# Optimization experiments

Measured on AMD Instinct MI355X. Metric: run time of the kernel, lower is better.

## Reference

```python
import jax, jax.numpy as jnp
import numpy as np

B, S, H, D = 4, 1024, 16, 64
DIM = H * D          # 1024
FF_INNER = 4 * DIM   # 4096
ROT_BASE = 1000.0


def _l2norm(x):
    # F.normalize(p=2, dim=-1): x / max(||x||_2, 1e-12)
    n = jnp.linalg.norm(x, axis=-1, keepdims=True)
    return x / jnp.maximum(n, 1e-12)


def _rmsnorm(x):
    return x * jax.lax.rsqrt(jnp.mean(x * x, axis=-1, keepdims=True) + jnp.finfo(jnp.float32).eps)


def _rope_tables(seq, d, base):
    inv_freq = base ** (-(jnp.arange(0, d, 2, dtype=jnp.float32) / d))
    freqs = jnp.outer(jnp.arange(seq, dtype=jnp.float32), inv_freq)  # [S, D/2]
    # original caches cos/sin in bfloat16
    cos = jnp.cos(freqs).astype(jnp.bfloat16)[None, :, None, :]
    sin = jnp.sin(freqs).astype(jnp.bfloat16)[None, :, None, :]
    return cos, sin


def _rope(x, cos, sin):
    d = x.shape[3] // 2
    x1, x2 = x[..., :d], x[..., d:]
    y1 = x1 * cos + x2 * sin
    y2 = -x1 * sin + x2 * cos
    return jnp.concatenate([y1, y2], axis=3).astype(x.dtype)


def setup_inputs() -> dict:
    key = jax.random.key(0)
    ks = jax.random.split(key, 12)
    w = lambda k, shp: 0.02 * jax.random.normal(k, shp, dtype=jnp.float32)
    inp = {
        'h_states': jax.random.normal(ks[0], (B, S, DIM), dtype=jnp.float32),
        'attention_mask': jnp.tril(jnp.ones((S, S), dtype=jnp.float32))[None].repeat(B, axis=0),
        'Wq': w(ks[1], (DIM, DIM)), 'Wk': w(ks[2], (DIM, DIM)), 'Wv': w(ks[3], (DIM, DIM)),
        'WqB': w(ks[4], (DIM, DIM)), 'WkB': w(ks[5], (DIM, DIM)),
        'Wo': w(ks[6], (DIM, DIM)), 'bo': jnp.zeros((DIM,), jnp.float32),
        'Wff_in': w(ks[7], (DIM, 2 * FF_INNER)), 'bff_in': jnp.zeros((2 * FF_INNER,), jnp.float32),
        'Wff_out': w(ks[8], (FF_INNER, DIM)), 'bff_out': jnp.zeros((DIM,), jnp.float32),
        'learnedlambda': jnp.asarray(1.0, jnp.float32),
        'l2normscale': jnp.log(jnp.asarray(float(S) ** 2 - float(S), jnp.float32)),
    }
    return inp


def reference(h_states, attention_mask, Wq, Wk, Wv, WqB, WkB, Wo, bo,
              Wff_in, bff_in, Wff_out, bff_out, learnedlambda, l2normscale):
    inner = _rmsnorm(h_states)                               # layerwisenorm (rmsnorm, no affine)
    scale = D ** -0.5

    def proj(Wm):
        return (inner @ Wm).reshape(B, S, H, D)
    q, k, v = proj(Wq), proj(Wk), proj(Wv)
    bq, bk = proj(WqB), proj(WkB)

    cos, sin = _rope_tables(S, D, ROT_BASE)
    q = _rope(_l2norm(q), cos, sin)
    k = _rope(_l2norm(k), cos, sin)
    bq = _rope(_l2norm(bq), cos, sin)
    bk = _rope(_l2norm(bk), cos, sin)

    # main branch: causal softmax attention, scale=1, scaled by learned l2normscale
    scores = jnp.einsum('bihd,bjhd->bhij', q, k)             # [B,H,S,S]
    causal = jnp.tril(jnp.ones((S, S), dtype=bool))
    scores = jnp.where(causal, scores, -jnp.inf)
    attn = jax.nn.softmax(scores, axis=-1)
    y = l2normscale * jnp.einsum('bhij,bjhd->bihd', attn, v)  # [B,S,H,D]

    # bias branch: softmax-free masked scores @ ones == row-sum broadcast over D
    bscores = jnp.einsum('bihd,bjhd->bhij', bq, bk) * scale
    bscores = bscores * attention_mask[:, None, :, :]
    brow = bscores.sum(axis=-1)                               # [B,H,S]
    y = y + jnp.transpose(brow, (0, 2, 1))[..., None]         # broadcast over D

    attn_out = y.reshape(B, S, DIM) @ Wo + bo

    # SwiGLU FFN: chunk -> x, gate; silu(gate) * x
    u = inner @ Wff_in + bff_in
    xh, gate = jnp.split(u, 2, axis=-1)
    dense_out = (jax.nn.silu(gate) * xh) @ Wff_out + bff_out

    return h_states * learnedlambda + dense_out + attn_out
```

## Files before the change

### kernel.cpp

```cpp
#include <hip/hip_runtime.h>
#include <stdint.h>
#include <math.h>

typedef float f32x4 __attribute__((ext_vector_type(4)));
typedef short s16x8 __attribute__((ext_vector_type(8)));
typedef unsigned short bfu;

#define AS1q const __attribute__((address_space(1))) void*
#define AS3q __attribute__((address_space(3))) void*

static __device__ __forceinline__ float bf2f(bfu v) {
  return __uint_as_float(((unsigned int)v) << 16);
}
static __device__ __forceinline__ bfu f2bf(float f) {
  unsigned int u = __float_as_uint(f);
  return (bfu)((u + 0x7fffu + ((u >> 16) & 1u)) >> 16);
}

struct PreArgs {
  const float* w5[5];
  const float* Wffin;
  const float* Wffout;
  const float* Wo;
  const float* h;
  bfu* wt5; bfu* wtfi; bfu* wtfoc;
  bfu* cosb; bfu* sinb; bfu* inner;
};
__global__ __launch_bounds__(256) void prologue_k(PreArgs a) {
  __shared__ float shmem[32 * 33];
  int id = blockIdx.x;
  if (id < 18432) {
    const float* W; bfu* Wt; int K, N, dstride, dofs, mode, nb, kb;
    if (id < 5120) {
      int z = id >> 10, rem = id & 1023;
      W = a.w5[z]; Wt = a.wt5 + ((size_t)z << 20);
      K = 1024; N = 1024; dstride = 1024; dofs = 0; mode = 0;
      nb = (rem & 31) << 5; kb = (rem >> 5) << 5;
    } else if (id < 13312) {
      int id2 = id - 5120;
      W = a.Wffin; Wt = a.wtfi; K = 1024; N = 8192; dstride = 1024; dofs = 0; mode = 1;
      nb = (id2 & 255) << 5; kb = (id2 >> 8) << 5;
    } else if (id < 17408) {
      int id3 = id - 13312;
      W = a.Wffout; Wt = a.wtfoc; K = 4096; N = 1024; dstride = 5120; dofs = 0; mode = 2;
      nb = (id3 & 31) << 5; kb = (id3 >> 5) << 5;
    } else {
      int id4 = id - 17408;
      W = a.Wo; Wt = a.wtfoc; K = 1024; N = 1024; dstride = 5120; dofs = 4096; mode = 2;
      nb = (id4 & 31) << 5; kb = (id4 >> 5) << 5;
    }
    float (*t)[33] = reinterpret_cast<float(*)[33]>(shmem);
    int tx = threadIdx.x & 31, ty = threadIdx.x >> 5;
#pragma unroll
    for (int i = 0; i < 4; i++) {
      int r = ty + i * 8;
      t[r][tx] = W[(size_t)(kb + r) * N + nb + tx];
    }
    __syncthreads();
#pragma unroll
    for (int i = 0; i < 4; i++) {
      int r = ty + i * 8;
      int n = nb + r;
      int nd = n;
      if (mode == 1) { int j = n & 4095, isg = n >> 12; nd = ((j >> 4) << 5) | (isg << 4) | (j & 15); }
      int k = kb + tx;
      int kp = (mode == 2) ? (((k >> 5) << 5) | ((k & 15) << 1) | ((k >> 4) & 1)) : k;
      Wt[(size_t)nd * dstride + dofs + kp] = f2bf(t[tx][r]);
    }
  } else if (id < 18560) {
    int idx = (id - 18432) * 256 + threadIdx.x;
    int s = idx >> 5, i = idx & 31;
    float f = powf(1000.0f, -(float)i / 32.0f);
    float fr = (float)s * f;
    a.cosb[idx] = f2bf(cosf(fr));
    a.sinb[idx] = f2bf(sinf(fr));
  } else {
    int row = id - 18560;
    const float* hr = a.h + (size_t)row * 1024;
    f32x4 x = *reinterpret_cast<const f32x4*>(hr + threadIdx.x * 4);
    float ss = x[0] * x[0] + x[1] * x[1] + x[2] * x[2] + x[3] * x[3];
    for (int off = 32; off; off >>= 1) ss += __shfl_down(ss, off);
    int wave = threadIdx.x >> 6, lane = threadIdx.x & 63;
    if (lane == 0) shmem[wave] = ss;
    __syncthreads();
    float tot = shmem[0] + shmem[1] + shmem[2] + shmem[3];
    float r = rsqrtf(tot * (1.0f / 1024.0f) + 1.1920929e-07f);
    bfu* o = a.inner + (size_t)row * 1024 + threadIdx.x * 4;
    o[0] = f2bf(x[0] * r); o[1] = f2bf(x[1] * r);
    o[2] = f2bf(x[2] * r); o[3] = f2bf(x[3] * r);
  }
}

template <int EPI>
__global__ __launch_bounds__(512, 2) void gemm256p(const bfu* __restrict__ A, const bfu* __restrict__ Bt,
                                                   bfu* __restrict__ outB,
                                                   const float* __restrict__ bias,
                                                   int M, int N, int K, int rbm, int rbn) {
  __shared__ __align__(16) char lds[131072];
  int nbx = N >> 8;
  int c = blockIdx.x & 7, rr = blockIdx.x >> 3;
  int ca = nbx / rbn;
  int bn0 = (c % ca) * rbn, bm0 = (c / ca) * rbm;
  int bm = bm0 + rr / rbn, bn = bn0 + rr % rbn;
  int tid = threadIdx.x, w = tid >> 6, lane = tid & 63;
  int wm = w >> 2, wn = w & 3;
  int g = lane >> 4, l15 = lane & 15;
  int NT = K >> 6;
  int NI = NT >> 1;

  f32x4 acc[8][4];
#pragma unroll
  for (int m = 0; m < 8; m++)
#pragma unroll
    for (int n = 0; n < 4; n++) acc[m][n] = (f32x4){0.f, 0.f, 0.f, 0.f};

  s16x8 af[4][2];
  s16x8 bfr[4][2];

  auto stage = [&](int mat, int kt, int hf) {
    if (kt >= NT) return;
    int d = kt & 1;
    const bfu* s0 = (mat == 0) ? A : Bt;
    int rowbase = ((mat == 0) ? bm : bn) * 256 + hf * 128;
    int k0 = kt << 6;
    char* base = lds + d * 65536 + mat * 32768 + hf * 16384;
#pragma unroll
    for (int r = 0; r < 2; r++) {
      int L = r * 512 + tid;
      int row = L >> 3, cc = L & 7;
      int kc = cc ^ (row & 7);
      const bfu* src = s0 + (size_t)(rowbase + row) * K + k0 + kc * 8;
      char* dst = base + r * 8192 + w * 1024;
      __builtin_amdgcn_global_load_lds((AS1q)src, (AS3q)dst, 16, 0, 0);
    }
  };

  auto ldA = [&](int d, int mh) {
    const char* base = lds + d * 65536 + wm * 16384;
#pragma unroll
    for (int mm = 0; mm < 4; mm++) {
      int row = mh * 64 + mm * 16 + l15;
#pragma unroll
      for (int ks = 0; ks < 2; ks++)
        af[mm][ks] = *reinterpret_cast<const s16x8*>(
            base + row * 128 + (((ks * 4 + g) ^ (row & 7)) << 4));
    }
  };
  auto ldB2 = [&](int d, int nh) {
    const char* base = lds + d * 65536 + 32768 + (wn >> 1) * 16384;
#pragma unroll
    for (int nn = 0; nn < 2; nn++) {
      int row = (wn & 1) * 64 + (nh * 2 + nn) * 16 + l15;
#pragma unroll
      for (int ks = 0; ks < 2; ks++)
        bfr[nh * 2 + nn][ks] = *reinterpret_cast<const s16x8*>(
            base + row * 128 + (((ks * 4 + g) ^ (row & 7)) << 4));
    }
  };
  auto mfma_q = [&](int mh, int nh) {
    asm volatile("s_waitcnt lgkmcnt(0)" ::: "memory");
    __builtin_amdgcn_sched_barrier(0);
    __builtin_amdgcn_s_barrier();
    __builtin_amdgcn_s_setprio(1);
#pragma unroll
    for (int mm = 0; mm < 4; mm++)
#pragma unroll
      for (int nn = 0; nn < 2; nn++) {
        int n = nh * 2 + nn, m = mh * 4 + mm;
#pragma unroll
        for (int ks = 0; ks < 2; ks++)
          acc[m][n] = __builtin_amdgcn_mfma_f32_16x16x32_bf16(af[mm][ks], bfr[n][ks], acc[m][n], 0, 0, 0);
      }
    __builtin_amdgcn_s_setprio(0);
    __builtin_amdgcn_sched_barrier(0);
  };

  stage(1, 0, 0); stage(0, 0, 0); stage(0, 0, 1); stage(1, 0, 1);
  stage(1, 1, 0); stage(1, 1, 1);
  asm volatile("s_waitcnt vmcnt(4)" ::: "memory");
  __builtin_amdgcn_s_barrier();
  __builtin_amdgcn_sched_barrier(0);

  for (int i = 0; i < NI; i++) {
    int t0 = 2 * i, t1 = 2 * i + 1;
    bool last = (i == NI - 1);
    ldA(0, 0); ldB2(0, 0);
    stage(0, t1, 0);
    mfma_q(0, 0);
    ldB2(0, 1);
    stage(0, t1, 1);
    mfma_q(0, 1);
    ldA(0, 1);
    stage(1, t0 + 2, 0);
    mfma_q(1, 0);
    stage(1, t0 + 2, 1);
    mfma_q(1, 1);
    if (last) { asm volatile("s_waitcnt vmcnt(0)" ::: "memory"); }
    else      { asm volatile("s_waitcnt vmcnt(4)" ::: "memory"); }
    __builtin_amdgcn_s_barrier();
    __builtin_amdgcn_sched_barrier(0);
    ldA(1, 0); ldB2(1, 0);
    stage(0, t0 + 2, 0);
    mfma_q(0, 0);
    ldB2(1, 1);
    stage(0, t0 + 2, 1);
    mfma_q(0, 1);
    ldA(1, 1);
    stage(1, t1 + 2, 0);
    mfma_q(1, 0);
    stage(1, t1 + 2, 1);
    mfma_q(1, 1);
    asm volatile("s_waitcnt vmcnt(4)" ::: "memory");
    __builtin_amdgcn_s_barrier();
    __builtin_amdgcn_sched_barrier(0);
  }

  int j0 = (bn * 8 + wn * 2) * 16 + l15;
  float bx0 = bias[j0], bg0 = bias[j0 + 4096];
  float bx1 = bias[j0 + 16], bg1 = bias[j0 + 16 + 4096];
  int cb = (bn * 4 + wn) * 32 + 2 * l15;
#pragma unroll
  for (int m = 0; m < 8; m++) {
#pragma unroll
    for (int r = 0; r < 4; r++) {
      int row = bm * 256 + wm * 128 + m * 16 + g * 4 + r;
      float xh0 = acc[m][0][r] + bx0, gt0 = acc[m][1][r] + bg0;
      float xh1 = acc[m][2][r] + bx1, gt1 = acc[m][3][r] + bg1;
      float s0 = gt0 / (1.0f + __expf(-gt0)) * xh0;
      float s1 = gt1 / (1.0f + __expf(-gt1)) * xh1;
      unsigned int pk = (unsigned int)f2bf(s0) | ((unsigned int)f2bf(s1) << 16);
      *reinterpret_cast<unsigned int*>(outB + (size_t)row * 5120 + cb) = pk;
    }
  }
}

__global__ __launch_bounds__(256, 3) void gemm128p(const bfu* __restrict__ A, const bfu* __restrict__ Bt,
                                                   bfu* __restrict__ qb, bfu* __restrict__ kb,
                                                   bfu* __restrict__ vT,
                                                   bfu* __restrict__ bqh, bfu* __restrict__ bkh,
                                                   const bfu* __restrict__ ct, const bfu* __restrict__ st,
                                                   int M, int N, int K, int rbm, int rbn) {
  __shared__ __align__(16) char lds[49152];
  int nbx = N >> 7;
  int c = blockIdx.x & 7, rr = blockIdx.x >> 3;
  int ca = nbx / rbn;
  int bn0 = (c % ca) * rbn, bm0 = (c / ca) * rbm;
  int bm = bm0 + rr / rbn, bn = bn0 + rr % rbn;
  int tid = threadIdx.x, w = tid >> 6, lane = tid & 63;
  int wm = w >> 1, wn = w & 1;
  int g = lane >> 4, l15 = lane & 15;
  int NT = K >> 5;

  f32x4 acc[4][4];
#pragma unroll
  for (int m = 0; m < 4; m++)
#pragma unroll
    for (int n = 0; n < 4; n++) acc[m][n] = (f32x4){0.f, 0.f, 0.f, 0.f};

  auto stage = [&](int buf, int t) {
    int k0 = t << 5;
#pragma unroll
    for (int r = 0; r < 2; r++) {
      int L = r * 256 + tid;
      int row = L >> 2, cc = L & 3;
      int kc = cc ^ (row & 3);
      const bfu* srcA = A + (size_t)(bm * 128 + row) * K + k0 + kc * 8;
      char* dstA = lds + buf * 16384 + r * 4096 + w * 1024;
      __builtin_amdgcn_global_load_lds((AS1q)srcA, (AS3q)dstA, 16, 0, 0);
      const bfu* srcB = Bt + (size_t)(bn * 128 + row) * K + k0 + kc * 8;
      char* dstB = lds + buf * 16384 + 8192 + r * 4096 + w * 1024;
      __builtin_amdgcn_global_load_lds((AS1q)srcB, (AS3q)dstB, 16, 0, 0);
    }
  };

  stage(0, 0); stage(1, 1);
  asm volatile("s_waitcnt vmcnt(4)" ::: "memory");
  __builtin_amdgcn_s_barrier();
  __builtin_amdgcn_sched_barrier(0);

  int bc = 0;
  for (int t = 0; t < NT; t++) {
    int bs = bc + 2; if (bs >= 3) bs -= 3;
    if (t + 2 < NT) stage(bs, t + 2);
    const char* la = lds + bc * 16384;
    const char* lb = la + 8192;
    s16x8 af[4], bfr[4];
#pragma unroll
    for (int m = 0; m < 4; m++) {
      int row = wm * 64 + m * 16 + l15;
      af[m] = *reinterpret_cast<const s16x8*>(la + row * 64 + ((g ^ (row & 3)) << 4));
    }
#pragma unroll
    for (int n = 0; n < 4; n++) {
      int row = wn * 64 + n * 16 + l15;
      bfr[n] = *reinterpret_cast<const s16x8*>(lb + row * 64 + ((g ^ (row & 3)) << 4));
    }
    asm volatile("s_waitcnt lgkmcnt(0)" ::: "memory");
    __builtin_amdgcn_sched_barrier(0);
    __builtin_amdgcn_s_setprio(1);
#pragma unroll
    for (int m = 0; m < 4; m++)
#pragma unroll
      for (int n = 0; n < 4; n++)
        acc[m][n] = __builtin_amdgcn_mfma_f32_16x16x32_bf16(af[m], bfr[n], acc[m][n], 0, 0, 0);
    __builtin_amdgcn_s_setprio(0);
    __builtin_amdgcn_sched_barrier(0);
    if (t < NT - 2) { asm volatile("s_waitcnt vmcnt(4)" ::: "memory"); }
    else            { asm volatile("s_waitcnt vmcnt(0)" ::: "memory"); }
    __builtin_amdgcn_s_barrier();
    __builtin_amdgcn_sched_barrier(0);
    bc++; if (bc == 3) bc = 0;
  }

  int which = bn >> 3;
  int hh = (bn & 7) * 2 + wn;
  if (which == 2) {
    bfu* lv = reinterpret_cast<bfu*>(lds);
#pragma unroll
    for (int m = 0; m < 4; m++) {
#pragma unroll
      for (int r = 0; r < 4; r++) {
        int sl = wm * 64 + m * 16 + g * 4 + r;
#pragma unroll
        for (int j = 0; j < 4; j++) {
          int d = j * 16 + l15;
          lv[(wn * 64 + d) * 136 + sl] = f2bf(acc[m][j][r]);
        }
      }
    }
    __syncthreads();
    int b = bm >> 3, h0 = (bn & 7) * 2;
#pragma unroll
    for (int i = 0; i < 8; i++) {
      int linear = i * 256 + tid;
      int hw = linear >> 10, rem = linear & 1023;
      int d = rem >> 4, sl8 = (rem & 15) << 3;
      s16x8 v8 = *reinterpret_cast<const s16x8*>(&lv[(hw * 64 + d) * 136 + sl8]);
      size_t dstofs = (((size_t)((b << 4) + h0 + hw) << 6) + d) * 1024 + (bm & 7) * 128 + sl8;
      *reinterpret_cast<s16x8*>(vT + dstofs) = v8;
    }
  } else {
#pragma unroll
    for (int m = 0; m < 4; m++) {
#pragma unroll
      for (int r = 0; r < 4; r++) {
        int row = bm * 128 + wm * 64 + m * 16 + g * 4 + r;
        int s = row & 1023, b = row >> 10;
        float a0 = acc[m][0][r], a1 = acc[m][1][r];
        float a2 = acc[m][2][r], a3 = acc[m][3][r];
        float ss = a0 * a0 + a1 * a1 + a2 * a2 + a3 * a3;
        ss += __shfl_xor(ss, 1); ss += __shfl_xor(ss, 2);
        ss += __shfl_xor(ss, 4); ss += __shfl_xor(ss, 8);
        float inv = 1.0f / fmaxf(sqrtf(ss), 1e-12f);
        float xn0 = a0 * inv, xn1 = a1 * inv, xn2 = a2 * inv, xn3 = a3 * inv;
        float c0 = bf2f(ct[(s << 5) + l15]),      s0v = bf2f(st[(s << 5) + l15]);
        float c1 = bf2f(ct[(s << 5) + 16 + l15]), s1v = bf2f(st[(s << 5) + 16 + l15]);
        float o0 = xn0 * c0 + xn2 * s0v;
        float o1 = xn1 * c1 + xn3 * s1v;
        float o2 = xn2 * c0 - xn0 * s0v;
        float o3 = xn3 * c1 - xn1 * s1v;
        unsigned long long pk =
            (unsigned long long)((unsigned int)f2bf(o0) | ((unsigned int)f2bf(o1) << 16)) |
            ((unsigned long long)((unsigned int)f2bf(o2) | ((unsigned int)f2bf(o3) << 16)) << 32);
        size_t base = ((((size_t)((b << 4) + hh) << 10) + s) << 6) + (l15 << 2);
        bfu* dst = (which == 0) ? qb : (which == 1) ? kb : (which == 3) ? bqh : bkh;
        *reinterpret_cast<unsigned long long*>(dst + base) = pk;
      }
    }
  }
}

__global__ __launch_bounds__(256, 3) void gemm128f(const bfu* __restrict__ A, const bfu* __restrict__ Bt,
                                                   float* __restrict__ out,
                                                   const float* __restrict__ b1,
                                                   const float* __restrict__ b2,
                                                   const float* __restrict__ lam,
                                                   const float* __restrict__ h,
                                                   int M, int N, int K, int rbm, int rbn) {
  __shared__ __align__(16) char lds[98304];
  int nbx = N >> 7;
  int c = blockIdx.x & 7, rr = blockIdx.x >> 3;
  int ca = nbx / rbn;
  int bn0 = (c % ca) * rbn, bm0 = (c / ca) * rbm;
  int bm = bm0 + rr / rbn, bn = bn0 + rr % rbn;
  int tid = threadIdx.x, w = tid >> 6, lane = tid & 63;
  int wm = w >> 1, wn = w & 1;
  int g = lane >> 4, l15 = lane & 15;
  int NT = K >> 6;

  f32x4 acc[4][4];
#pragma unroll
  for (int m = 0; m < 4; m++)
#pragma unroll
    for (int n = 0; n < 4; n++) acc[m][n] = (f32x4){0.f, 0.f, 0.f, 0.f};

  auto stage = [&](int buf, int t) {
    int k0 = t << 6;
#pragma unroll
    for (int r = 0; r < 4; r++) {
      int L = r * 256 + tid;
      int row = L >> 3, cc = L & 7;
      int kc = cc ^ (row & 7);
      const bfu* srcA = A + (size_t)(bm * 128 + row) * K + k0 + kc * 8;
      char* dstA = lds + buf * 32768 + r * 4096 + w * 1024;
      __builtin_amdgcn_global_load_lds((AS1q)srcA, (AS3q)dstA, 16, 0, 0);
    }
#pragma unroll
    for (int r = 0; r < 4; r++) {
      int L = r * 256 + tid;
      int row = L >> 3, cc = L & 7;
      int kc = cc ^ (row & 7);
      const bfu* srcB = Bt + (size_t)(bn * 128 + row) * K + k0 + kc * 8;
      char* dstB = lds + buf * 32768 + 16384 + r * 4096 + w * 1024;
      __builtin_amdgcn_global_load_lds((AS1q)srcB, (AS3q)dstB, 16, 0, 0);
    }
  };

  stage(0, 0); stage(1, 1);
  asm volatile("s_waitcnt vmcnt(8)" ::: "memory");
  __builtin_amdgcn_s_barrier();
  __builtin_amdgcn_sched_barrier(0);

  int bc = 0;
  for (int t = 0; t < NT; t++) {
    int bs = bc + 2; if (bs >= 3) bs -= 3;
    if (t + 2 < NT) stage(bs, t + 2);
    const char* la = lds + bc * 32768;
    const char* lb = la + 16384;
    s16x8 af[4][2], bfr[4][2];
#pragma unroll
    for (int m = 0; m < 4; m++) {
      int row = wm * 64 + m * 16 + l15;
#pragma unroll
      for (int ks = 0; ks < 2; ks++)
        af[m][ks] = *reinterpret_cast<const s16x8*>(
            la + row * 128 + (((ks * 4 + g) ^ (row & 7)) << 4));
    }
#pragma unroll
    for (int n = 0; n < 4; n++) {
      int row = wn * 64 + n * 16 + l15;
#pragma unroll
      for (int ks = 0; ks < 2; ks++)
        bfr[n][ks] = *reinterpret_cast<const s16x8*>(
            lb + row * 128 + (((ks * 4 + g) ^ (row & 7)) << 4));
    }
    asm volatile("s_waitcnt lgkmcnt(0)" ::: "memory");
    __builtin_amdgcn_sched_barrier(0);
    __builtin_amdgcn_s_setprio(1);
#pragma unroll
    for (int m = 0; m < 4; m++)
#pragma unroll
      for (int n = 0; n < 4; n++)
#pragma unroll
        for (int ks = 0; ks < 2; ks++)
          acc[m][n] = __builtin_amdgcn_mfma_f32_16x16x32_bf16(af[m][ks], bfr[n][ks], acc[m][n], 0, 0, 0);
    __builtin_amdgcn_s_setprio(0);
    __builtin_amdgcn_sched_barrier(0);
    if (t < NT - 2) { asm volatile("s_waitcnt vmcnt(8)" ::: "memory"); }
    else            { asm volatile("s_waitcnt vmcnt(0)" ::: "memory"); }
    __builtin_amdgcn_s_barrier();
    __builtin_amdgcn_sched_barrier(0);
    bc++; if (bc == 3) bc = 0;
  }

  float lv = lam[0];
#pragma unroll
  for (int m = 0; m < 4; m++) {
    int row = bm * 128 + wm * 64 + m * 16 + g * 4;
#pragma unroll
    for (int n = 0; n < 4; n++) {
      int col = bn * 128 + wn * 64 + n * 16 + l15;
      float bb = b1[col] + b2[col];
#pragma unroll
      for (int r = 0; r < 4; r++) {
        size_t o = (size_t)(row + r) * 1024 + col;
        out[o] = acc[m][n][r] + bb + lv * h[o];
      }
    }
  }
}

__global__ __launch_bounds__(512) void brow_all(const bfu* __restrict__ bq, const bfu* __restrict__ bk,
                                                float* __restrict__ brow) {
  __shared__ float csums[8][64];
  int bh = blockIdx.x;
  int wave = threadIdx.x >> 6, lane = threadIdx.x & 63;
  size_t base = ((size_t)bh * 1024 + wave * 128) * 64 + lane;
  float s = 0.f;
  for (int j = 0; j < 128; j++) s += bf2f(bk[base + (size_t)j * 64]);
  csums[wave][lane] = s;
  __syncthreads();
  float p = 0.f;
  for (int cc = 0; cc < wave; cc++) p += csums[cc][lane];
  for (int j = 0; j < 128; j++) {
    p += bf2f(bk[base + (size_t)j * 64]);
    float t = bf2f(bq[base + (size_t)j * 64]) * p;
#pragma unroll
    for (int m2 = 1; m2 < 64; m2 <<= 1) t += __shfl_xor(t, m2);
    if (lane == 0) brow[bh * 1024 + wave * 128 + j] = 0.125f * t;
  }
}

__global__ __launch_bounds__(256) void flash_k(const bfu* __restrict__ q, const bfu* __restrict__ k,
                                               const bfu* __restrict__ vT,
                                               const float* __restrict__ brow,
                                               const float* __restrict__ l2p,
                                               bfu* __restrict__ y) {
  __shared__ __align__(16) bfu P[4][2][16][72];
  int id = blockIdx.x;
  int sub = id & 255;
  int qt = (id >> 8) ? 7 - (sub >> 6) : (sub >> 6);
  int bh = sub & 63;
  int wave = threadIdx.x >> 6, lane = threadIdx.x & 63;
  int g = lane >> 4, l15 = lane & 15;
  const size_t bhofs = (size_t)bh << 16;
  int rt0 = qt * 128 + wave * 32;

  s16x8 aq[2][2];
#pragma unroll
  for (int m = 0; m < 2; m++)
#pragma unroll
    for (int ks = 0; ks < 2; ks++)
      aq[m][ks] = *reinterpret_cast<const s16x8*>(
          q + bhofs + (size_t)(rt0 + m * 16 + l15) * 64 + ks * 32 + g * 8);

  f32x4 O[2][4];
  float mr[2][4], lr[2][4];
#pragma unroll
  for (int m = 0; m < 2; m++)
#pragma unroll
    for (int r = 0; r < 4; r++) { O[m][r] = (f32x4){0.f, 0.f, 0.f, 0.f}; mr[m][r] = -3.0e38f; lr[m][r] = 0.f; }

  s16x8 kA[4][2], kB[4][2];
  auto loadK = [&](s16x8 (&kd)[4][2], int jt) {
#pragma unroll
    for (int nt = 0; nt < 4; nt++)
#pragma unroll
      for (int ks = 0; ks < 2; ks++)
        kd[nt][ks] = *reinterpret_cast<const s16x8*>(
            k + bhofs + (size_t)(jt * 64 + nt * 16 + l15) * 64 + ks * 32 + g * 8);
  };

  int njt = 2 * qt + 2;
  loadK(kA, 0);

  auto body = [&](int jt, s16x8 (&kc)[4][2], s16x8 (&kn)[4][2], bool pf) {
    s16x8 vv[4][2];
#pragma unroll
    for (int nt = 0; nt < 4; nt++)
#pragma unroll
      for (int ks = 0; ks < 2; ks++)
        vv[nt][ks] = *reinterpret_cast<const s16x8*>(
            vT + ((size_t)(bh * 64 + nt * 16 + l15) << 10) + jt * 64 + ks * 32 + g * 8);

    bool act[2] = { jt * 64 <= rt0 + 15, jt * 64 <= rt0 + 31 };
    f32x4 sfr[2][4];
#pragma unroll
    for (int m = 0; m < 2; m++) {
      if (!act[m]) continue;
#pragma unroll
      for (int nt = 0; nt < 4; nt++) {
        sfr[m][nt] = (f32x4){0.f, 0.f, 0.f, 0.f};
#pragma unroll
        for (int ks = 0; ks < 2; ks++)
          sfr[m][nt] = __builtin_amdgcn_mfma_f32_16x16x32_bf16(aq[m][ks], kc[nt][ks], sfr[m][nt], 0, 0, 0);
      }
    }
    if (pf) loadK(kn, jt + 1);

#pragma unroll
    for (int m = 0; m < 2; m++) {
      if (!act[m]) continue;
      int rtm = rt0 + m * 16;
      if (jt * 64 + 63 > rtm) {
#pragma unroll
        for (int ntn = 0; ntn < 4; ntn++)
#pragma unroll
          for (int r = 0; r < 4; r++)
            if (jt * 64 + ntn * 16 + l15 > rtm + g * 4 + r) sfr[m][ntn][r] = -1e30f;
      }
      float alpha[4];
#pragma unroll
      for (int r = 0; r < 4; r++) {
        float v = fmaxf(fmaxf(sfr[m][0][r], sfr[m][1][r]), fmaxf(sfr[m][2][r], sfr[m][3][r]));
#pragma unroll
        for (int m2 = 1; m2 < 16; m2 <<= 1) v = fmaxf(v, __shfl_xor(v, m2));
        float mn = fmaxf(mr[m][r], v);
        alpha[r] = __expf(mr[m][r] - mn);
        mr[m][r] = mn;
      }
#pragma unroll
      for (int r = 0; r < 4; r++) {
        float rs = 0.f;
#pragma unroll
        for (int ntn = 0; ntn < 4; ntn++) {
          float e = __expf(sfr[m][ntn][r] - mr[m][r]);
          rs += e;
          P[wave][m][g * 4 + r][ntn * 16 + l15] = f2bf(e);
        }
#pragma unroll
        for (int m2 = 1; m2 < 16; m2 <<= 1) rs += __shfl_xor(rs, m2);
        lr[m][r] = lr[m][r] * alpha[r] + rs;
#pragma unroll
        for (int ntn = 0; ntn < 4; ntn++) O[m][ntn][r] *= alpha[r];
      }
    }
    asm volatile("s_waitcnt lgkmcnt(0)" ::: "memory");
    __builtin_amdgcn_sched_barrier(0);
#pragma unroll
    for (int m = 0; m < 2; m++) {
      if (!act[m]) continue;
      s16x8 pa[2];
#pragma unroll
      for (int ks = 0; ks < 2; ks++)
        pa[ks] = *reinterpret_cast<const s16x8*>(&P[wave][m][l15][ks * 32 + g * 8]);
#pragma unroll
      for (int nt = 0; nt < 4; nt++)
#pragma unroll
        for (int ks = 0; ks < 2; ks++)
          O[m][nt] = __builtin_amdgcn_mfma_f32_16x16x32_bf16(pa[ks], vv[nt][ks], O[m][nt], 0, 0, 0);
    }
  };

  for (int jt = 0; jt < njt; jt += 2) {
    body(jt, kA, kB, true);
    body(jt + 1, kB, kA, jt + 2 < njt);
  }

  float l2ns = l2p[0];
  int b = bh >> 4, hq = bh & 15;
#pragma unroll
  for (int m = 0; m < 2; m++)
#pragma unroll
    for (int r = 0; r < 4; r++) {
      int rowg = rt0 + m * 16 + g * 4 + r;
      float br = brow[bh * 1024 + rowg];
      float sc = l2ns / lr[m][r];
      float v0 = O[m][0][r] * sc + br;
      float v1 = O[m][1][r] * sc + br;
      float v2 = O[m][2][r] * sc + br;
      float v3 = O[m][3][r] * sc + br;
      unsigned int p01 = (unsigned int)f2bf(v0) | ((unsigned int)f2bf(v1) << 16);
      unsigned int p23 = (unsigned int)f2bf(v2) | ((unsigned int)f2bf(v3) << 16);
      size_t base = (size_t)(b * 1024 + rowg) * 5120 + 4096 + hq * 64;
      *reinterpret_cast<unsigned int*>(y + base + 2 * l15) = p01;
      *reinterpret_cast<unsigned int*>(y + base + 32 + 2 * l15) = p23;
    }
}

extern "C" void kernel_launch(void* const* d_in, const int* in_sizes, int n_in,
                              void* d_out, int out_size, void* d_ws, size_t ws_size,
                              hipStream_t stream) {
  const float* h      = (const float*)d_in[0];
  const float* Wq     = (const float*)d_in[2];
  const float* Wk     = (const float*)d_in[3];
  const float* Wv     = (const float*)d_in[4];
  const float* WqB    = (const float*)d_in[5];
  const float* WkB    = (const float*)d_in[6];
  const float* Wo     = (const float*)d_in[7];
  const float* bo     = (const float*)d_in[8];
  const float* Wffin  = (const float*)d_in[9];
  const float* bffin  = (const float*)d_in[10];
  const float* Wffout = (const float*)d_in[11];
  const float* bffout = (const float*)d_in[12];
  const float* lam    = (const float*)d_in[13];
  const float* l2ns   = (const float*)d_in[14];
  float* out = (float*)d_out;

  char* ws = (char*)d_ws;
  size_t off = 0;
  auto alloc = [&](size_t bytes) { void* p = ws + off; off += bytes; return p; };
  bfu* wt5   = (bfu*)alloc(5ull * 1024 * 1024 * 2);
  bfu* wtfi  = (bfu*)alloc(8192ull * 1024 * 2);
  bfu* wtfoc = (bfu*)alloc(1024ull * 5120 * 2);
  bfu* cosb  = (bfu*)alloc(1024ull * 32 * 2);
  bfu* sinb  = (bfu*)alloc(1024ull * 32 * 2);
  bfu* inner = (bfu*)alloc(4096ull * 1024 * 2);
  bfu* qb    = (bfu*)alloc(64ull * 1024 * 64 * 2);
  bfu* kb    = (bfu*)alloc(64ull * 1024 * 64 * 2);
  bfu* vtb   = (bfu*)alloc(64ull * 1024 * 64 * 2);
  bfu* bqh   = (bfu*)alloc(64ull * 1024 * 64 * 2);
  bfu* bkh   = (bfu*)alloc(64ull * 1024 * 64 * 2);
  float* browb = (float*)alloc(64ull * 1024 * 4);
  bfu* AB    = (bfu*)alloc(4096ull * 5120 * 2);

  PreArgs pa;
  pa.w5[0] = Wq; pa.w5[1] = Wk; pa.w5[2] = Wv; pa.w5[3] = WqB; pa.w5[4] = WkB;
  pa.Wffin = Wffin; pa.Wffout = Wffout; pa.Wo = Wo; pa.h = h;
  pa.wt5 = wt5; pa.wtfi = wtfi; pa.wtfoc = wtfoc;
  pa.cosb = cosb; pa.sinb = sinb; pa.inner = inner;
  prologue_k<<<dim3(22656), 256, 0, stream>>>(pa);

  gemm128p<<<dim3(1280), 256, 0, stream>>>(inner, wt5, qb, kb, vtb, bqh, bkh, cosb, sinb,
                                           4096, 5120, 1024, 32, 5);

  brow_all<<<dim3(64), 512, 0, stream>>>(bqh, bkh, browb);

  flash_k<<<dim3(512), 256, 0, stream>>>(qb, kb, vtb, browb, l2ns, AB);

  gemm256p<1><<<dim3(512), 512, 0, stream>>>(inner, wtfi, AB, bffin,
                                             4096, 8192, 1024, 8, 8);

  gemm128f<<<dim3(256), 256, 0, stream>>>(AB, wtfoc, out, bffout, bo, lam, h,
                                          4096, 1024, 5120, 8, 4);
}
```

Baseline: 322.6 us.

## Halve flash attention query tile to 64 rows and double grid size

The flash attention kernel now gives each wave 16 query rows instead of 32, so a block covers 64 rows and the grid doubles to 1024 blocks. Query tiles are ordered in a four-way zigzag to balance causal work. This raises parallelism and shrinks the per-wave register footprint and causal-mask waste. In exchange each block loads K and V for half as many query rows, which doubles K/V traffic per unit of work.

```diff
diff --git a/kernel.cpp b/kernel.cpp
--- a/kernel.cpp
+++ b/kernel.cpp
@@ -506,30 +506,27 @@
                                                const float* __restrict__ brow,
                                                const float* __restrict__ l2p,
                                                bfu* __restrict__ y) {
-  __shared__ __align__(16) bfu P[4][2][16][72];
+  __shared__ __align__(16) bfu P[4][16][72];
   int id = blockIdx.x;
   int sub = id & 255;
-  int qt = (id >> 8) ? 7 - (sub >> 6) : (sub >> 6);
-  int bh = sub & 63;
+  int a = sub >> 6, bh = sub & 63;
+  int quad = id >> 8;
+  int qt = (quad == 0) ? a : (quad == 1) ? 7 - a : (quad == 2) ? 8 + a : 15 - a;
   int wave = threadIdx.x >> 6, lane = threadIdx.x & 63;
   int g = lane >> 4, l15 = lane & 15;
   const size_t bhofs = (size_t)bh << 16;
-  int rt0 = qt * 128 + wave * 32;
-
-  s16x8 aq[2][2];
-#pragma unroll
-  for (int m = 0; m < 2; m++)
-#pragma unroll
-    for (int ks = 0; ks < 2; ks++)
-      aq[m][ks] = *reinterpret_cast<const s16x8*>(
-          q + bhofs + (size_t)(rt0 + m * 16 + l15) * 64 + ks * 32 + g * 8);
-
-  f32x4 O[2][4];
-  float mr[2][4], lr[2][4];
-#pragma unroll
-  for (int m = 0; m < 2; m++)
-#pragma unroll
-    for (int r = 0; r < 4; r++) { O[m][r] = (f32x4){0.f, 0.f, 0.f, 0.f}; mr[m][r] = -3.0e38f; lr[m][r] = 0.f; }
+  int rt0 = qt * 64 + wave * 16;
+
+  s16x8 aq[2];
+#pragma unroll
+  for (int ks = 0; ks < 2; ks++)
+    aq[ks] = *reinterpret_cast<const s16x8*>(
+        q + bhofs + (size_t)(rt0 + l15) * 64 + ks * 32 + g * 8);
+
+  f32x4 O[4];
+  float mr[4], lr[4];
+#pragma unroll
+  for (int r = 0; r < 4; r++) { O[r] = (f32x4){0.f, 0.f, 0.f, 0.f}; mr[r] = -3.0e38f; lr[r] = 0.f; }
 
   s16x8 kA[4][2], kB[4][2];
   auto loadK = [&](s16x8 (&kd)[4][2], int jt) {
@@ -541,7 +538,7 @@
             k + bhofs + (size_t)(jt * 64 + nt * 16 + l15) * 64 + ks * 32 + g * 8);
   };
 
-  int njt = 2 * qt + 2;
+  int njt = qt + 1;
   loadK(kA, 0);
 
   auto body = [&](int jt, s16x8 (&kc)[4][2], s16x8 (&kn)[4][2], bool pf) {
@@ -553,99 +550,83 @@
         vv[nt][ks] = *reinterpret_cast<const s16x8*>(
             vT + ((size_t)(bh * 64 + nt * 16 + l15) << 10) + jt * 64 + ks * 32 + g * 8);
 
-    bool act[2] = { jt * 64 <= rt0 + 15, jt * 64 <= rt0 + 31 };
-    f32x4 sfr[2][4];
-#pragma unroll
-    for (int m = 0; m < 2; m++) {
-      if (!act[m]) continue;
-#pragma unroll
-      for (int nt = 0; nt < 4; nt++) {
-        sfr[m][nt] = (f32x4){0.f, 0.f, 0.f, 0.f};
-#pragma unroll
-        for (int ks = 0; ks < 2; ks++)
-          sfr[m][nt] = __builtin_amdgcn_mfma_f32_16x16x32_bf16(aq[m][ks], kc[nt][ks], sfr[m][nt], 0, 0, 0);
+    f32x4 sfr[4];
+#pragma unroll
+    for (int nt = 0; nt < 4; nt++) {
+      sfr[nt] = (f32x4){0.f, 0.f, 0.f, 0.f};
+#pragma unroll
+      for (int ks = 0; ks < 2; ks++)
+        sfr[nt] = __builtin_amdgcn_mfma_f32_16x16x32_bf16(aq[ks], kc[nt][ks], sfr[nt], 0, 0, 0);
+    }
+    if (pf) loadK(kn, jt + 1);
+
+    if (jt == qt) {
+#pragma unroll
+      for (int ntn = 0; ntn < 4; ntn++)
+#pragma unroll
+        for (int r = 0; r < 4; r++)
+          if (jt * 64 + ntn * 16 + l15 > rt0 + g * 4 + r) sfr[ntn][r] = -1e30f;
+    }
+    float alpha[4];
+#pragma unroll
+    for (int r = 0; r < 4; r++) {
+      float v = fmaxf(fmaxf(sfr[0][r], sfr[1][r]), fmaxf(sfr[2][r], sfr[3][r]));
+#pragma unroll
+      for (int m2 = 1; m2 < 16; m2 <<= 1) v = fmaxf(v, __shfl_xor(v, m2));
+      float mn = fmaxf(mr[r], v);
+      alpha[r] = __expf(mr[r] - mn);
+      mr[r] = mn;
+    }
+#pragma unroll
+    for (int r = 0; r < 4; r++) {
+      float rs = 0.f;
+#pragma unroll
+      for (int ntn = 0; ntn < 4; ntn++) {
+        float e = __expf(sfr[ntn][r] - mr[r]);
+        rs += e;
+        P[wave][g * 4 + r][ntn * 16 + l15] = f2bf(e);
       }
-    }
-    if (pf) loadK(kn, jt + 1);
-
-#pragma unroll
-    for (int m = 0; m < 2; m++) {
-      if (!act[m]) continue;
-      int rtm = rt0 + m * 16;
-      if (jt * 64 + 63 > rtm) {
-#pragma unroll
-        for (int ntn = 0; ntn < 4; ntn++)
-#pragma unroll
-          for (int r = 0; r < 4; r++)
-            if (jt * 64 + ntn * 16 + l15 > rtm + g * 4 + r) sfr[m][ntn][r] = -1e30f;
-      }
-      float alpha[4];
-#pragma unroll
-      for (int r = 0; r < 4; r++) {
-        float v = fmaxf(fmaxf(sfr[m][0][r], sfr[m][1][r]), fmaxf(sfr[m][2][r], sfr[m][3][r]));
-#pragma unroll
-        for (int m2 = 1; m2 < 16; m2 <<= 1) v = fmaxf(v, __shfl_xor(v, m2));
-        float mn = fmaxf(mr[m][r], v);
-        alpha[r] = __expf(mr[m][r] - mn);
-        mr[m][r] = mn;
-      }
-#pragma unroll
-      for (int r = 0; r < 4; r++) {
-        float rs = 0.f;
-#pragma unroll
-        for (int ntn = 0; ntn < 4; ntn++) {
-          float e = __expf(sfr[m][ntn][r] - mr[m][r]);
-          rs += e;
-          P[wave][m][g * 4 + r][ntn * 16 + l15] = f2bf(e);
-        }
-#pragma unroll
-        for (int m2 = 1; m2 < 16; m2 <<= 1) rs += __shfl_xor(rs, m2);
-        lr[m][r] = lr[m][r] * alpha[r] + rs;
-#pragma unroll
-        for (int ntn = 0; ntn < 4; ntn++) O[m][ntn][r] *= alpha[r];
-      }
+#pragma unroll
+      for (int m2 = 1; m2 < 16; m2 <<= 1) rs += __shfl_xor(rs, m2);
+      lr[r] = lr[r] * alpha[r] + rs;
+#pragma unroll
+      for (int ntn = 0; ntn < 4; ntn++) O[ntn][r] *= alpha[r];
     }
     asm volatile("s_waitcnt lgkmcnt(0)" ::: "memory");
     __builtin_amdgcn_sched_barrier(0);
-#pragma unroll
-    for (int m = 0; m < 2; m++) {
-      if (!act[m]) continue;
-      s16x8 pa[2];
-#pragma unroll
-      for (int ks = 0; ks < 2; ks++)
-        pa[ks] = *reinterpret_cast<const s16x8*>(&P[wave][m][l15][ks * 32 + g * 8]);
-#pragma unroll
-      for (int nt = 0; nt < 4; nt++)
-#pragma unroll
-        for (int ks = 0; ks < 2; ks++)
-          O[m][nt] = __builtin_amdgcn_mfma_f32_16x16x32_bf16(pa[ks], vv[nt][ks], O[m][nt], 0, 0, 0);
-    }
-  };
-
-  for (int jt = 0; jt < njt; jt += 2) {
-    body(jt, kA, kB, true);
-    body(jt + 1, kB, kA, jt + 2 < njt);
+    s16x8 pa[2];
+#pragma unroll
+    for (int ks = 0; ks < 2; ks++)
+      pa[ks] = *reinterpret_cast<const s16x8*>(&P[wave][l15][ks * 32 + g * 8]);
+#pragma unroll
+    for (int nt = 0; nt < 4; nt++)
+#pragma unroll
+      for (int ks = 0; ks < 2; ks++)
+        O[nt] = __builtin_amdgcn_mfma_f32_16x16x32_bf16(pa[ks], vv[nt][ks], O[nt], 0, 0, 0);
+  };
+
+  for (int jt = 0; jt < njt; jt++) {
+    if (jt & 1) body(jt, kB, kA, jt + 1 < njt);
+    else        body(jt, kA, kB, jt + 1 < njt);
   }
 
   float l2ns = l2p[0];
   int b = bh >> 4, hq = bh & 15;
 #pragma unroll
-  for (int m = 0; m < 2; m++)
-#pragma unroll
-    for (int r = 0; r < 4; r++) {
-      int rowg = rt0 + m * 16 + g * 4 + r;
-      float br = brow[bh * 1024 + rowg];
-      float sc = l2ns / lr[m][r];
-      float v0 = O[m][0][r] * sc + br;
-      float v1 = O[m][1][r] * sc + br;
-      float v2 = O[m][2][r] * sc + br;
-      float v3 = O[m][3][r] * sc + br;
-      unsigned int p01 = (unsigned int)f2bf(v0) | ((unsigned int)f2bf(v1) << 16);
-      unsigned int p23 = (unsigned int)f2bf(v2) | ((unsigned int)f2bf(v3) << 16);
-      size_t base = (size_t)(b * 1024 + rowg) * 5120 + 4096 + hq * 64;
-      *reinterpret_cast<unsigned int*>(y + base + 2 * l15) = p01;
-      *reinterpret_cast<unsigned int*>(y + base + 32 + 2 * l15) = p23;
-    }
+  for (int r = 0; r < 4; r++) {
+    int rowg = rt0 + g * 4 + r;
+    float br = brow[bh * 1024 + rowg];
+    float sc = l2ns / lr[r];
+    float v0 = O[0][r] * sc + br;
+    float v1 = O[1][r] * sc + br;
+    float v2 = O[2][r] * sc + br;
+    float v3 = O[3][r] * sc + br;
+    unsigned int p01 = (unsigned int)f2bf(v0) | ((unsigned int)f2bf(v1) << 16);
+    unsigned int p23 = (unsigned int)f2bf(v2) | ((unsigned int)f2bf(v3) << 16);
+    size_t base = (size_t)(b * 1024 + rowg) * 5120 + 4096 + hq * 64;
+    *reinterpret_cast<unsigned int*>(y + base + 2 * l15) = p01;
+    *reinterpret_cast<unsigned int*>(y + base + 32 + 2 * l15) = p23;
+  }
 }
 
 extern "C" void kernel_launch(void* const* d_in, const int* in_sizes, int n_in,
@@ -696,7 +677,7 @@
 
   brow_all<<<dim3(64), 512, 0, stream>>>(bqh, bkh, browb);
 
-  flash_k<<<dim3(512), 256, 0, stream>>>(qb, kb, vtb, browb, l2ns, AB);
+  flash_k<<<dim3(1024), 256, 0, stream>>>(qb, kb, vtb, browb, l2ns, AB);
 
   gemm256p<1><<<dim3(512), 512, 0, stream>>>(inner, wtfi, AB, bffin,
                                              4096, 8192, 1024, 8, 8);
```

Measured after the change: 338.3 us. 4.9% more time.

## Merge flash attention and SwiGLU FFN-in GEMM into one heterogeneous launch

Applied to the files above, without the earlier changes.

Replaces the separate flash attention kernel and the FFN-in GEMM with one kernel launch. The first 256 blocks each run two former flash blocks, one per group of four waves, and the remaining 512 blocks run the 256x256 SwiGLU GEMM with its tile sizes hardcoded. Both branches write disjoint column ranges of the shared AB buffer, so the two independent stages can overlap on the device and the tail of one can fill idle CUs left by the other. In exchange, the flash blocks now run at 512 threads with the GEMM's 128KB LDS allocation and launch bounds, which may lower their occupancy or raise register pressure.

```diff
diff --git a/kernel.cpp b/kernel.cpp
--- a/kernel.cpp
+++ b/kernel.cpp
@@ -91,22 +91,166 @@
   }
 }
 
-template <int EPI>
-__global__ __launch_bounds__(512, 2) void gemm256p(const bfu* __restrict__ A, const bfu* __restrict__ Bt,
-                                                   bfu* __restrict__ outB,
-                                                   const float* __restrict__ bias,
-                                                   int M, int N, int K, int rbm, int rbn) {
+__global__ __launch_bounds__(512, 2) void fused_k(const bfu* __restrict__ q, const bfu* __restrict__ k,
+                                                  const bfu* __restrict__ vT,
+                                                  const float* __restrict__ brow,
+                                                  const float* __restrict__ l2p,
+                                                  const bfu* __restrict__ A, const bfu* __restrict__ Bt,
+                                                  bfu* __restrict__ AB,
+                                                  const float* __restrict__ bias) {
   __shared__ __align__(16) char lds[131072];
-  int nbx = N >> 8;
-  int c = blockIdx.x & 7, rr = blockIdx.x >> 3;
-  int ca = nbx / rbn;
-  int bn0 = (c % ca) * rbn, bm0 = (c / ca) * rbm;
-  int bm = bm0 + rr / rbn, bn = bn0 + rr % rbn;
   int tid = threadIdx.x, w = tid >> 6, lane = tid & 63;
+  int g = lane >> 4, l15 = lane & 15;
+
+  if (blockIdx.x < 256) {
+    int fid = blockIdx.x + ((w >> 2) << 8);
+    int sub = fid & 255;
+    int qt = (fid >> 8) ? 7 - (sub >> 6) : (sub >> 6);
+    int bh = sub & 63;
+    const size_t bhofs = (size_t)bh << 16;
+    int rt0 = qt * 128 + (w & 3) * 32;
+    bfu* P = reinterpret_cast<bfu*>(lds) + (size_t)w * (2 * 16 * 72);
+
+    s16x8 aq[2][2];
+#pragma unroll
+    for (int m = 0; m < 2; m++)
+#pragma unroll
+      for (int ks = 0; ks < 2; ks++)
+        aq[m][ks] = *reinterpret_cast<const s16x8*>(
+            q + bhofs + (size_t)(rt0 + m * 16 + l15) * 64 + ks * 32 + g * 8);
+
+    f32x4 O[2][4];
+    float mr[2][4], lr[2][4];
+#pragma unroll
+    for (int m = 0; m < 2; m++)
+#pragma unroll
+      for (int r = 0; r < 4; r++) { O[m][r] = (f32x4){0.f, 0.f, 0.f, 0.f}; mr[m][r] = -3.0e38f; lr[m][r] = 0.f; }
+
+    s16x8 kA[4][2], kB[4][2];
+    auto loadK = [&](s16x8 (&kd)[4][2], int jt) {
+#pragma unroll
+      for (int nt = 0; nt < 4; nt++)
+#pragma unroll
+        for (int ks = 0; ks < 2; ks++)
+          kd[nt][ks] = *reinterpret_cast<const s16x8*>(
+              k + bhofs + (size_t)(jt * 64 + nt * 16 + l15) * 64 + ks * 32 + g * 8);
+    };
+
+    int njt = 2 * qt + 2;
+    loadK(kA, 0);
+
+    auto body = [&](int jt, s16x8 (&kc)[4][2], s16x8 (&kn)[4][2], bool pf) {
+      s16x8 vv[4][2];
+#pragma unroll
+      for (int nt = 0; nt < 4; nt++)
+#pragma unroll
+        for (int ks = 0; ks < 2; ks++)
+          vv[nt][ks] = *reinterpret_cast<const s16x8*>(
+              vT + ((size_t)(bh * 64 + nt * 16 + l15) << 10) + jt * 64 + ks * 32 + g * 8);
+
+      bool act[2] = { jt * 64 <= rt0 + 15, jt * 64 <= rt0 + 31 };
+      f32x4 sfr[2][4];
+#pragma unroll
+      for (int m = 0; m < 2; m++) {
+        if (!act[m]) continue;
+#pragma unroll
+        for (int nt = 0; nt < 4; nt++) {
+          sfr[m][nt] = (f32x4){0.f, 0.f, 0.f, 0.f};
+#pragma unroll
+          for (int ks = 0; ks < 2; ks++)
+            sfr[m][nt] = __builtin_amdgcn_mfma_f32_16x16x32_bf16(aq[m][ks], kc[nt][ks], sfr[m][nt], 0, 0, 0);
+        }
+      }
+      if (pf) loadK(kn, jt + 1);
+
+#pragma unroll
+      for (int m = 0; m < 2; m++) {
+        if (!act[m]) continue;
+        int rtm = rt0 + m * 16;
+        if (jt * 64 + 63 > rtm) {
+#pragma unroll
+          for (int ntn = 0; ntn < 4; ntn++)
+#pragma unroll
+            for (int r = 0; r < 4; r++)
+              if (jt * 64 + ntn * 16 + l15 > rtm + g * 4 + r) sfr[m][ntn][r] = -1e30f;
+        }
+        float alpha[4];
+#pragma unroll
+        for (int r = 0; r < 4; r++) {
+          float v = fmaxf(fmaxf(sfr[m][0][r], sfr[m][1][r]), fmaxf(sfr[m][2][r], sfr[m][3][r]));
+#pragma unroll
+          for (int m2 = 1; m2 < 16; m2 <<= 1) v = fmaxf(v, __shfl_xor(v, m2));
+          float mn = fmaxf(mr[m][r], v);
+          alpha[r] = __expf(mr[m][r] - mn);
+          mr[m][r] = mn;
+        }
+#pragma unroll
+        for (int r = 0; r < 4; r++) {
+          float rs = 0.f;
+#pragma unroll
+          for (int ntn = 0; ntn < 4; ntn++) {
+            float e = __expf(sfr[m][ntn][r] - mr[m][r]);
+            rs += e;
+            P[(m * 16 + g * 4 + r) * 72 + ntn * 16 + l15] = f2bf(e);
+          }
+#pragma unroll
+          for (int m2 = 1; m2 < 16; m2 <<= 1) rs += __shfl_xor(rs, m2);
+          lr[m][r] = lr[m][r] * alpha[r] + rs;
+#pragma unroll
+          for (int ntn = 0; ntn < 4; ntn++) O[m][ntn][r] *= alpha[r];
+        }
+      }
+      asm volatile("s_waitcnt lgkmcnt(0)" ::: "memory");
+      __builtin_amdgcn_sched_barrier(0);
+#pragma unroll
+      for (int m = 0; m < 2; m++) {
+        if (!act[m]) continue;
+        s16x8 pa[2];
+#pragma unroll
+        for (int ks = 0; ks < 2; ks++)
+          pa[ks] = *reinterpret_cast<const s16x8*>(&P[(m * 16 + l15) * 72 + ks * 32 + g * 8]);
+#pragma unroll
+        for (int nt = 0; nt < 4; nt++)
+#pragma unroll
+          for (int ks = 0; ks < 2; ks++)
+            O[m][nt] = __builtin_amdgcn_mfma_f32_16x16x32_bf16(pa[ks], vv[nt][ks], O[m][nt], 0, 0, 0);
+      }
+    };
+
+    for (int jt = 0; jt < njt; jt += 2) {
+      body(jt, kA, kB, true);
+      body(jt + 1, kB, kA, jt + 2 < njt);
+    }
+
+    float l2ns = l2p[0];
+    int b = bh >> 4, hq = bh & 15;
+#pragma unroll
+    for (int m = 0; m < 2; m++)
+#pragma unroll
+      for (int r = 0; r < 4; r++) {
+        int rowg = rt0 + m * 16 + g * 4 + r;
+        float br = brow[bh * 1024 + rowg];
+        float sc = l2ns / lr[m][r];
+        float v0 = O[m][0][r] * sc + br;
+        float v1 = O[m][1][r] * sc + br;
+        float v2 = O[m][2][r] * sc + br;
+        float v3 = O[m][3][r] * sc + br;
+        unsigned int p01 = (unsigned int)f2bf(v0) | ((unsigned int)f2bf(v1) << 16);
+        unsigned int p23 = (unsigned int)f2bf(v2) | ((unsigned int)f2bf(v3) << 16);
+        size_t base = (size_t)(b * 1024 + rowg) * 5120 + 4096 + hq * 64;
+        *reinterpret_cast<unsigned int*>(AB + base + 2 * l15) = p01;
+        *reinterpret_cast<unsigned int*>(AB + base + 32 + 2 * l15) = p23;
+      }
+    return;
+  }
+
+  int id0 = blockIdx.x - 256;
+  int c = id0 & 7, rr = id0 >> 3;
+  int bn0 = (c & 3) * 8, bm0 = (c >> 2) * 8;
+  int bm = bm0 + rr / 8, bn = bn0 + rr % 8;
   int wm = w >> 2, wn = w & 3;
-  int g = lane >> 4, l15 = lane & 15;
-  int NT = K >> 6;
-  int NI = NT >> 1;
+  const int K = 1024;
+  const int NT = 16, NI = 8;
 
   f32x4 acc[8][4];
 #pragma unroll
@@ -229,7 +373,7 @@
       float s0 = gt0 / (1.0f + __expf(-gt0)) * xh0;
       float s1 = gt1 / (1.0f + __expf(-gt1)) * xh1;
       unsigned int pk = (unsigned int)f2bf(s0) | ((unsigned int)f2bf(s1) << 16);
-      *reinterpret_cast<unsigned int*>(outB + (size_t)row * 5120 + cb) = pk;
+      *reinterpret_cast<unsigned int*>(AB + (size_t)row * 5120 + cb) = pk;
     }
   }
 }
@@ -501,153 +645,6 @@
   }
 }
 
-__global__ __launch_bounds__(256) void flash_k(const bfu* __restrict__ q, const bfu* __restrict__ k,
-                                               const bfu* __restrict__ vT,
-                                               const float* __restrict__ brow,
-                                               const float* __restrict__ l2p,
-                                               bfu* __restrict__ y) {
-  __shared__ __align__(16) bfu P[4][2][16][72];
-  int id = blockIdx.x;
-  int sub = id & 255;
-  int qt = (id >> 8) ? 7 - (sub >> 6) : (sub >> 6);
-  int bh = sub & 63;
-  int wave = threadIdx.x >> 6, lane = threadIdx.x & 63;
-  int g = lane >> 4, l15 = lane & 15;
-  const size_t bhofs = (size_t)bh << 16;
-  int rt0 = qt * 128 + wave * 32;
-
-  s16x8 aq[2][2];
-#pragma unroll
-  for (int m = 0; m < 2; m++)
-#pragma unroll
-    for (int ks = 0; ks < 2; ks++)
-      aq[m][ks] = *reinterpret_cast<const s16x8*>(
-          q + bhofs + (size_t)(rt0 + m * 16 + l15) * 64 + ks * 32 + g * 8);
-
-  f32x4 O[2][4];
-  float mr[2][4], lr[2][4];
-#pragma unroll
-  for (int m = 0; m < 2; m++)
-#pragma unroll
-    for (int r = 0; r < 4; r++) { O[m][r] = (f32x4){0.f, 0.f, 0.f, 0.f}; mr[m][r] = -3.0e38f; lr[m][r] = 0.f; }
-
-  s16x8 kA[4][2], kB[4][2];
-  auto loadK = [&](s16x8 (&kd)[4][2], int jt) {
-#pragma unroll
-    for (int nt = 0; nt < 4; nt++)
-#pragma unroll
-      for (int ks = 0; ks < 2; ks++)
-        kd[nt][ks] = *reinterpret_cast<const s16x8*>(
-            k + bhofs + (size_t)(jt * 64 + nt * 16 + l15) * 64 + ks * 32 + g * 8);
-  };
-
-  int njt = 2 * qt + 2;
-  loadK(kA, 0);
-
-  auto body = [&](int jt, s16x8 (&kc)[4][2], s16x8 (&kn)[4][2], bool pf) {
-    s16x8 vv[4][2];
-#pragma unroll
-    for (int nt = 0; nt < 4; nt++)
-#pragma unroll
-      for (int ks = 0; ks < 2; ks++)
-        vv[nt][ks] = *reinterpret_cast<const s16x8*>(
-            vT + ((size_t)(bh * 64 + nt * 16 + l15) << 10) + jt * 64 + ks * 32 + g * 8);
-
-    bool act[2] = { jt * 64 <= rt0 + 15, jt * 64 <= rt0 + 31 };
-    f32x4 sfr[2][4];
-#pragma unroll
-    for (int m = 0; m < 2; m++) {
-      if (!act[m]) continue;
-#pragma unroll
-      for (int nt = 0; nt < 4; nt++) {
-        sfr[m][nt] = (f32x4){0.f, 0.f, 0.f, 0.f};
-#pragma unroll
-        for (int ks = 0; ks < 2; ks++)
-          sfr[m][nt] = __builtin_amdgcn_mfma_f32_16x16x32_bf16(aq[m][ks], kc[nt][ks], sfr[m][nt], 0, 0, 0);
-      }
-    }
-    if (pf) loadK(kn, jt + 1);
-
-#pragma unroll
-    for (int m = 0; m < 2; m++) {
-      if (!act[m]) continue;
-      int rtm = rt0 + m * 16;
-      if (jt * 64 + 63 > rtm) {
-#pragma unroll
-        for (int ntn = 0; ntn < 4; ntn++)
-#pragma unroll
-          for (int r = 0; r < 4; r++)
-            if (jt * 64 + ntn * 16 + l15 > rtm + g * 4 + r) sfr[m][ntn][r] = -1e30f;
-      }
-      float alpha[4];
-#pragma unroll
-      for (int r = 0; r < 4; r++) {
-        float v = fmaxf(fmaxf(sfr[m][0][r], sfr[m][1][r]), fmaxf(sfr[m][2][r], sfr[m][3][r]));
-#pragma unroll
-        for (int m2 = 1; m2 < 16; m2 <<= 1) v = fmaxf(v, __shfl_xor(v, m2));
-        float mn = fmaxf(mr[m][r], v);
-        alpha[r] = __expf(mr[m][r] - mn);
-        mr[m][r] = mn;
-      }
-#pragma unroll
-      for (int r = 0; r < 4; r++) {
-        float rs = 0.f;
-#pragma unroll
-        for (int ntn = 0; ntn < 4; ntn++) {
-          float e = __expf(sfr[m][ntn][r] - mr[m][r]);
-          rs += e;
-          P[wave][m][g * 4 + r][ntn * 16 + l15] = f2bf(e);
-        }
-#pragma unroll
-        for (int m2 = 1; m2 < 16; m2 <<= 1) rs += __shfl_xor(rs, m2);
-        lr[m][r] = lr[m][r] * alpha[r] + rs;
-#pragma unroll
-        for (int ntn = 0; ntn < 4; ntn++) O[m][ntn][r] *= alpha[r];
-      }
-    }
-    asm volatile("s_waitcnt lgkmcnt(0)" ::: "memory");
-    __builtin_amdgcn_sched_barrier(0);
-#pragma unroll
-    for (int m = 0; m < 2; m++) {
-      if (!act[m]) continue;
-      s16x8 pa[2];
-#pragma unroll
-      for (int ks = 0; ks < 2; ks++)
-        pa[ks] = *reinterpret_cast<const s16x8*>(&P[wave][m][l15][ks * 32 + g * 8]);
-#pragma unroll
-      for (int nt = 0; nt < 4; nt++)
-#pragma unroll
-        for (int ks = 0; ks < 2; ks++)
-          O[m][nt] = __builtin_amdgcn_mfma_f32_16x16x32_bf16(pa[ks], vv[nt][ks], O[m][nt], 0, 0, 0);
-    }
-  };
-
-  for (int jt = 0; jt < njt; jt += 2) {
-    body(jt, kA, kB, true);
-    body(jt + 1, kB, kA, jt + 2 < njt);
-  }
-
-  float l2ns = l2p[0];
-  int b = bh >> 4, hq = bh & 15;
-#pragma unroll
-  for (int m = 0; m < 2; m++)
-#pragma unroll
-    for (int r = 0; r < 4; r++) {
-      int rowg = rt0 + m * 16 + g * 4 + r;
-      float br = brow[bh * 1024 + rowg];
-      float sc = l2ns / lr[m][r];
-      float v0 = O[m][0][r] * sc + br;
-      float v1 = O[m][1][r] * sc + br;
-      float v2 = O[m][2][r] * sc + br;
-      float v3 = O[m][3][r] * sc + br;
-      unsigned int p01 = (unsigned int)f2bf(v0) | ((unsigned int)f2bf(v1) << 16);
-      unsigned int p23 = (unsigned int)f2bf(v2) | ((unsigned int)f2bf(v3) << 16);
-      size_t base = (size_t)(b * 1024 + rowg) * 5120 + 4096 + hq * 64;
-      *reinterpret_cast<unsigned int*>(y + base + 2 * l15) = p01;
-      *reinterpret_cast<unsigned int*>(y + base + 32 + 2 * l15) = p23;
-    }
-}
-
 extern "C" void kernel_launch(void* const* d_in, const int* in_sizes, int n_in,
                               void* d_out, int out_size, void* d_ws, size_t ws_size,
                               hipStream_t stream) {
@@ -696,10 +693,8 @@
 
   brow_all<<<dim3(64), 512, 0, stream>>>(bqh, bkh, browb);
 
-  flash_k<<<dim3(512), 256, 0, stream>>>(qb, kb, vtb, browb, l2ns, AB);
-
-  gemm256p<1><<<dim3(512), 512, 0, stream>>>(inner, wtfi, AB, bffin,
-                                             4096, 8192, 1024, 8, 8);
+  fused_k<<<dim3(768), 512, 0, stream>>>(qb, kb, vtb, browb, l2ns,
+                                         inner, wtfi, AB, bffin);
 
   gemm128f<<<dim3(256), 256, 0, stream>>>(AB, wtfoc, out, bffout, bo, lam, h,
                                           4096, 1024, 5120, 8, 4);
```

Result: faster. 304.6 us, median of 2 (-5.6%).
